# Optimization experiments

Hardware: AMD Instinct MI355X
Metric: run time of the kernel (lower is better)

The kernel has to match this reference:

```python
import jax, jax.numpy as jnp
import numpy as np

D_MODEL = 1024
N_HEADS = 16
HEAD_DIM = 64
INNER = N_HEADS * HEAD_DIM
D_FF = 4096


def ln_novar(x, w, b):
    # mean-only 'layernorm' (no variance division), per original LayerNormNoVar
    u = jnp.mean(x, axis=-1, keepdims=True)
    return w * (x - u) + b


def setup_inputs() -> dict:
    key = jax.random.key(0)
    ks = jax.random.split(key, 12)
    s = lambda k, shape, scale: jax.random.normal(k, shape, dtype=jnp.float32) * scale
    inp = {
        "src": s(ks[0], (4, 2048, D_MODEL), 1.0),
        "pre_norm_w": jnp.ones((D_MODEL,), jnp.float32),
        "pre_norm_b": jnp.zeros((D_MODEL,), jnp.float32),
        "wq": s(ks[1], (D_MODEL, INNER), 0.02),
        "wk": s(ks[2], (D_MODEL, INNER), 0.02),
        "wv": s(ks[3], (D_MODEL, INNER), 0.02),
        "w_proj": s(ks[4], (INNER, D_MODEL), 0.02),
        "b_proj": jnp.zeros((D_MODEL,), jnp.float32),
        "norm1_w": jnp.ones((D_MODEL,), jnp.float32),
        "norm1_b": jnp.zeros((D_MODEL,), jnp.float32),
        "w1": s(ks[5], (D_MODEL, D_FF), 0.02),
        "b1": jnp.zeros((D_FF,), jnp.float32),
        "w2": s(ks[6], (D_FF, D_MODEL), 0.02),
        "b2": jnp.zeros((D_MODEL,), jnp.float32),
    }
    return inp


def reference(src, pre_norm_w, pre_norm_b, wq, wk, wv, w_proj, b_proj,
              norm1_w, norm1_b, w1, b1, w2, b2):
    B, N, _ = src.shape
    scale = HEAD_DIM ** -0.5
    x = ln_novar(src, pre_norm_w, pre_norm_b)
    q = (x @ wq).reshape(B, N, N_HEADS, HEAD_DIM)
    k = (x @ wk).reshape(B, N, N_HEADS, HEAD_DIM)
    v = (x @ wv).reshape(B, N, N_HEADS, HEAD_DIM)
    attn = jnp.einsum('bqhd,bkhd->bhqk', q, k) * scale
    attn = jax.nn.softmax(attn, axis=-1)
    o = jnp.einsum('bhqk,bkhd->bqhd', attn, v).reshape(B, N, INNER)
    o = o @ w_proj + b_proj
    src = src + o
    src = ln_novar(src, norm1_w, norm1_b)
    ff = jax.nn.relu(src @ w1 + b1) @ w2 + b2
    return src + ff
```

## Files before the change

### kernel.cpp

```cpp
#include <hip/hip_runtime.h>
#include <hip/hip_bf16.h>
#include <stdint.h>

typedef __hip_bfloat16 bf16;
typedef float f32x4 __attribute__((ext_vector_type(4)));
typedef float f32x16 __attribute__((ext_vector_type(16)));
typedef short v8s __attribute__((ext_vector_type(8)));
typedef __bf16 v8bf __attribute__((ext_vector_type(8)));
typedef unsigned int v4u __attribute__((ext_vector_type(4)));
typedef unsigned int u32;

static constexpr int MROWS = 8192;
static constexpr int DM    = 1024;
static constexpr int DFF   = 4096;
static constexpr int SEQ   = 2048;

__device__ __forceinline__ f32x4 mfma16(v8s a, v8s b, f32x4 c) {
  return __builtin_amdgcn_mfma_f32_16x16x32_bf16(
      __builtin_bit_cast(v8bf, a), __builtin_bit_cast(v8bf, b), c, 0, 0, 0);
}
__device__ __forceinline__ f32x16 mfma32(v8s a, v8s b, f32x16 c) {
  return __builtin_amdgcn_mfma_f32_32x32x16_bf16(
      __builtin_bit_cast(v8bf, a), __builtin_bit_cast(v8bf, b), c, 0, 0, 0);
}

__device__ __forceinline__ void gload_lds16(const void* g, void* l) {
  __builtin_amdgcn_global_load_lds(
      (const __attribute__((address_space(1))) void*)g,
      (__attribute__((address_space(3))) void*)l, 16, 0, 0);
}

__device__ __forceinline__ u32 cvtpk_bf16(float a, float b) {
  u32 r;
  asm("v_cvt_pk_bf16_f32 %0, %1, %2" : "=v"(r) : "v"(a), "v"(b));
  return r;
}
__device__ __forceinline__ void pl32swap(u32& x, u32& y) {
  asm volatile("v_permlane32_swap_b32 %0, %1" : "+v"(x), "+v"(y));
}
__device__ __forceinline__ float fast_exp2(float x) {
  float r;
  asm("v_exp_f32 %0, %1" : "=v"(r) : "v"(x));
  return r;
}

__global__ __launch_bounds__(256) void transpose_cast(
    const float* __restrict__ W, bf16* __restrict__ WT, int K, int N) {
  __shared__ float tile[32][33];
  const int c0 = blockIdx.x * 32;
  const int r0 = blockIdx.y * 32;
  const int tx = threadIdx.x & 31, ty = threadIdx.x >> 5;
  #pragma unroll
  for (int i = 0; i < 32; i += 8)
    tile[ty + i][tx] = W[(size_t)(r0 + ty + i) * N + c0 + tx];
  __syncthreads();
  #pragma unroll
  for (int i = 0; i < 32; i += 8)
    WT[(size_t)(c0 + ty + i) * K + r0 + tx] = __float2bfloat16(tile[tx][ty + i]);
}

__global__ __launch_bounds__(256) void ln_novar_kernel(
    const float* __restrict__ x, const float* __restrict__ w,
    const float* __restrict__ b, bf16* __restrict__ ob, float* __restrict__ of) {
  const int row = blockIdx.x;
  const int t = threadIdx.x;
  const float4 v = ((const float4*)(x + (size_t)row * DM))[t];
  float s = v.x + v.y + v.z + v.w;
  #pragma unroll
  for (int off = 32; off > 0; off >>= 1) s += __shfl_down(s, off, 64);
  __shared__ float wsum[4];
  if ((t & 63) == 0) wsum[t >> 6] = s;
  __syncthreads();
  const float u = (wsum[0] + wsum[1] + wsum[2] + wsum[3]) * (1.0f / DM);
  const float4 wv = ((const float4*)w)[t];
  const float4 bv = ((const float4*)b)[t];
  const float o0 = wv.x * (v.x - u) + bv.x;
  const float o1 = wv.y * (v.y - u) + bv.y;
  const float o2 = wv.z * (v.z - u) + bv.z;
  const float o3 = wv.w * (v.w - u) + bv.w;
  bf16* op = ob + (size_t)row * DM + t * 4;
  op[0] = __float2bfloat16(o0); op[1] = __float2bfloat16(o1);
  op[2] = __float2bfloat16(o2); op[3] = __float2bfloat16(o3);
  if (of) {
    float4 o4; o4.x = o0; o4.y = o1; o4.z = o2; o4.w = o3;
    ((float4*)(of + (size_t)row * DM))[t] = o4;
  }
}

#define BM 128
#define BN 256
#define BK 64
#define ASZ (BM * BK)
#define BSZ (BN * BK)
template <int EPI>
__global__ __launch_bounds__(512, 2) void gemm_bt(
    const bf16* __restrict__ A, const bf16* __restrict__ BT,
    bf16* __restrict__ Cb, float* __restrict__ Cf,
    const float* __restrict__ bias, const float* __restrict__ res,
    int M, int Nn, int K) {
  __shared__ __align__(16) bf16 S[3][ASZ + BSZ];

  const int tid = threadIdx.x;
  const int lane = tid & 63;
  const int wave = tid >> 6;
  const int wr = wave >> 2;
  const int wcn = wave & 3;

  const int nwg = gridDim.x;
  const int nbx = Nn / BN;
  int bid = (blockIdx.x & 7) * (nwg >> 3) + (blockIdx.x >> 3);
  const int GM = 4;
  const int grp = bid / (GM * nbx);
  const int rem = bid - grp * (GM * nbx);
  const int by = grp * GM + (rem & (GM - 1));
  const int bx = rem >> 2;
  const int tM = by * BM, tN = bx * BN;

  f32x4 acc[4][4] = {};
  const int nk = K / BK;

  auto STAGE = [&](int buf, int kt) {
    const int k0 = kt * BK;
    bf16* Ab = &S[buf][0];
    bf16* Bb = &S[buf][ASZ];
    #pragma unroll
    for (int c = 0; c < 2; ++c) {
      const int slot = c * 512 + tid;
      const int row = slot >> 3, s = slot & 7;
      const int kk = ((s ^ (row & 7)) << 3);
      gload_lds16(A + (size_t)(tM + row) * K + k0 + kk, (void*)(Ab + slot * 8));
    }
    #pragma unroll
    for (int c = 0; c < 4; ++c) {
      const int slot = c * 512 + tid;
      const int row = slot >> 3, s = slot & 7;
      const int kk = ((s ^ (row & 7)) << 3);
      gload_lds16(BT + (size_t)(tN + row) * K + k0 + kk, (void*)(Bb + slot * 8));
    }
  };

  auto LD = [&](v8s* af, v8s* bfr, int buf, int kk) {
    const bf16* Ab = &S[buf][0];
    const bf16* Bb = &S[buf][ASZ];
    const int kslot = kk * 4 + (lane >> 4);
    #pragma unroll
    for (int m = 0; m < 4; ++m) {
      const int row = wr * 64 + m * 16 + (lane & 15);
      af[m] = *(const v8s*)(Ab + (row * 8 + (kslot ^ (row & 7))) * 8);
    }
    #pragma unroll
    for (int n = 0; n < 4; ++n) {
      const int row = wcn * 64 + n * 16 + (lane & 15);
      bfr[n] = *(const v8s*)(Bb + (row * 8 + (kslot ^ (row & 7))) * 8);
    }
  };

  v8s fA0[4], fB0[4], fA1[4], fB1[4];

  STAGE(0, 0);
  STAGE(1, 1);
  asm volatile("s_waitcnt vmcnt(6)" ::: "memory");
  __builtin_amdgcn_s_barrier();
  asm volatile("" ::: "memory");
  LD(fA0, fB0, 0, 0);

  for (int kt = 0; kt < nk; ++kt) {
    const int cur = kt % 3;
    if (kt + 2 < nk) STAGE((kt + 2) % 3, kt + 2);

    LD(fA1, fB1, cur, 1);
    __builtin_amdgcn_s_setprio(1);
    #pragma unroll
    for (int m = 0; m < 4; ++m)
      #pragma unroll
      for (int n = 0; n < 4; ++n)
        acc[m][n] = mfma16(fA0[m], fB0[n], acc[m][n]);
    __builtin_amdgcn_s_setprio(0);

    if (kt + 2 < nk) asm volatile("s_waitcnt vmcnt(6)" ::: "memory");
    else             asm volatile("s_waitcnt vmcnt(0)" ::: "memory");
    __builtin_amdgcn_s_barrier();
    asm volatile("" ::: "memory");

    if (kt + 1 < nk) LD(fA0, fB0, (kt + 1) % 3, 0);
    __builtin_amdgcn_s_setprio(1);
    #pragma unroll
    for (int m = 0; m < 4; ++m)
      #pragma unroll
      for (int n = 0; n < 4; ++n)
        acc[m][n] = mfma16(fA1[m], fB1[n], acc[m][n]);
    __builtin_amdgcn_s_setprio(0);

    asm volatile("" ::: "memory");
    __builtin_amdgcn_s_barrier();
    asm volatile("" ::: "memory");
  }

  #pragma unroll
  for (int m = 0; m < 4; ++m) {
    #pragma unroll
    for (int n = 0; n < 4; ++n) {
      const int row0 = tM + wr * 64 + m * 16 + ((lane >> 4) << 2);
      const int col = tN + wcn * 64 + n * 16 + (lane & 15);
      #pragma unroll
      for (int r = 0; r < 4; ++r) {
        const int row = row0 + r;
        float v = acc[m][n][r];
        if (EPI == 0) {
          Cb[(size_t)row * Nn + col] = __float2bfloat16(v);
        } else if (EPI == 1) {
          v += bias[col];
          v = fmaxf(v, 0.0f);
          Cb[(size_t)row * Nn + col] = __float2bfloat16(v);
        } else if (EPI == 2) {
          v += bias[col] + res[(size_t)row * Nn + col];
          Cf[(size_t)row * Nn + col] = v;
        } else {
          const int sec = tN >> 10;
          if (sec == 0) {
            Cb[(size_t)row * Nn + col] = __float2bfloat16(v);
          } else {
            const int b = row >> 11, nn2 = row & 2047;
            const int ktt = nn2 >> 6, key = nn2 & 63;
            if (sec == 1) {
              const int ck = col - 1024;
              const int h = ck >> 6, dc = (ck >> 3) & 7, e = ck & 7;
              bf16* krp = (bf16*)(void*)bias;
              krp[((size_t)((b * 16 + h) * 32 + ktt)) * 4096 + dc * 512 +
                  key * 8 + e] = __float2bfloat16(v);
            } else {
              const int cv = col - 2048;
              const int h = cv >> 6, d = cv & 63;
              const int kc = key >> 3, e2 = key & 7;
              bf16* vrp = (bf16*)(void*)res;
              vrp[((size_t)((b * 16 + h) * 32 + ktt)) * 4096 + kc * 512 +
                  d * 8 + e2] = __float2bfloat16(v);
            }
          }
        }
      }
    }
  }
}

#define PPV(i) ((i) < 16 ? s0[(i) & 15] : s1[(i) & 15])
__global__ __launch_bounds__(256, 4) void attn_kernel(
    const bf16* __restrict__ qkv, const bf16* __restrict__ krep,
    const bf16* __restrict__ vrep, bf16* __restrict__ ob) {
  const int qt = blockIdx.x & 15;
  const int bh = blockIdx.x >> 4;
  const int b = bh >> 4, h = bh & 15;
  const int tid = threadIdx.x;
  const int lane = tid & 63, wave = tid >> 6;
  const int c = lane & 31, hi = lane >> 5;
  const float CEXP = 0.180336880111120426f;

  __shared__ __align__(16) bf16 Ks[2][4096];
  __shared__ __align__(16) bf16 Vs[2][4096];

  const int qrow = qt * 128 + wave * 32 + c;
  const bf16* qp = qkv + (size_t)(b * SEQ + qrow) * 3072 + h * 64;
  v8s qf[4];
  #pragma unroll
  for (int ks = 0; ks < 4; ++ks)
    qf[ks] = *(const v8s*)(qp + ks * 16 + hi * 8);

  f32x16 o0 = {}, o1 = {};
  float mrow = -1e30f, lrow = 0.0f;

  const size_t tilebase = (size_t)(bh * 32) * 4096;
  #pragma unroll
  for (int j = 0; j < 2; ++j) {
    gload_lds16(krep + tilebase + (tid + j * 256) * 8, &Ks[0][(tid + j * 256) * 8]);
    gload_lds16(vrep + tilebase + (tid + j * 256) * 8, &Vs[0][(tid + j * 256) * 8]);
  }
  asm volatile("s_waitcnt vmcnt(0)" ::: "memory");
  __builtin_amdgcn_s_barrier();
  asm volatile("" ::: "memory");

  for (int kt = 0; kt < 32; ++kt) {
    const int cur = kt & 1;
    if (kt < 31) {
      const size_t nb = tilebase + (size_t)(kt + 1) * 4096;
      #pragma unroll
      for (int j = 0; j < 2; ++j) {
        gload_lds16(krep + nb + (tid + j * 256) * 8, &Ks[cur ^ 1][(tid + j * 256) * 8]);
        gload_lds16(vrep + nb + (tid + j * 256) * 8, &Vs[cur ^ 1][(tid + j * 256) * 8]);
      }
    }
    const bf16* KB = Ks[cur];
    const bf16* VB = Vs[cur];

    f32x16 s0 = {}, s1 = {};
    __builtin_amdgcn_s_setprio(1);
    #pragma unroll
    for (int ks = 0; ks < 4; ++ks) {
      const int ch = (2 * ks + hi) * 512;
      v8s a0 = *(const v8s*)(KB + ch + c * 8);
      v8s a1 = *(const v8s*)(KB + ch + (c + 32) * 8);
      s0 = mfma32(a0, qf[ks], s0);
      s1 = mfma32(a1, qf[ks], s1);
    }
    __builtin_amdgcn_s_setprio(0);

    float mA = -1e30f, mB = -1e30f;
    #pragma unroll
    for (int i = 0; i < 16; i += 2) {
      mA = fmaxf(fmaxf(s0[i], s0[i + 1]), mA);
      mB = fmaxf(fmaxf(s1[i], s1[i + 1]), mB);
    }
    float tmax = fmaxf(mA, mB);
    tmax = fmaxf(tmax, __shfl_xor(tmax, 32, 64));
    if (__any(tmax - mrow > 64.0f)) {
      const float mnew = fmaxf(mrow, tmax);
      const float ef = fast_exp2((mrow - mnew) * CEXP);
      mrow = mnew;
      lrow *= ef;
      #pragma unroll
      for (int r = 0; r < 16; ++r) {
        const float efq = __shfl(ef, (r & 3) + 8 * (r >> 2) + 4 * hi, 64);
        o0[r] *= efq;
        o1[r] *= efq;
      }
    }
    const float nmc = -mrow * CEXP;
    float rs0 = 0.0f, rs1 = 0.0f;
    #pragma unroll
    for (int i = 0; i < 16; ++i) {
      s0[i] = fast_exp2(fmaf(s0[i], CEXP, nmc));
      s1[i] = fast_exp2(fmaf(s1[i], CEXP, nmc));
      rs0 += s0[i];
      rs1 += s1[i];
    }
    float rs = rs0 + rs1;
    rs += __shfl_xor(rs, 32, 64);
    lrow += rs;

    v8s pa[4];
    #pragma unroll
    for (int ks = 0; ks < 4; ++ks) {
      u32 x  = cvtpk_bf16(PPV(8 * ks + 0), PPV(8 * ks + 1));
      u32 y  = cvtpk_bf16(PPV(8 * ks + 4), PPV(8 * ks + 5));
      u32 x2 = cvtpk_bf16(PPV(8 * ks + 2), PPV(8 * ks + 3));
      u32 y2 = cvtpk_bf16(PPV(8 * ks + 6), PPV(8 * ks + 7));
      pl32swap(x, y);
      pl32swap(x2, y2);
      v4u w; w.x = x; w.y = x2; w.z = y; w.w = y2;
      pa[ks] = __builtin_bit_cast(v8s, w);
    }

    __builtin_amdgcn_s_setprio(1);
    #pragma unroll
    for (int ks = 0; ks < 4; ++ks) {
      const int ch = (2 * ks + hi) * 512;
      v8s b0 = *(const v8s*)(VB + ch + c * 8);
      v8s b1 = *(const v8s*)(VB + ch + (c + 32) * 8);
      o0 = mfma32(pa[ks], b0, o0);
      o1 = mfma32(pa[ks], b1, o1);
    }
    __builtin_amdgcn_s_setprio(0);

    asm volatile("s_waitcnt vmcnt(0)" ::: "memory");
    __builtin_amdgcn_s_barrier();
    asm volatile("" ::: "memory");
  }

  const float rl = 1.0f / lrow;
  const size_t orow0 = (size_t)(b * SEQ + qt * 128 + wave * 32);
  #pragma unroll
  for (int r = 0; r < 16; ++r) {
    const int q = (r & 3) + 8 * (r >> 2) + 4 * hi;
    const float rq = __shfl(rl, q, 64);
    bf16* op = ob + (orow0 + q) * DM + h * 64;
    op[c] = __float2bfloat16(o0[r] * rq);
    op[32 + c] = __float2bfloat16(o1[r] * rq);
  }
}

extern "C" void kernel_launch(void* const* d_in, const int* in_sizes, int n_in,
                              void* d_out, int out_size, void* d_ws,
                              size_t ws_size, hipStream_t stream) {
  const float* src   = (const float*)d_in[0];
  const float* pnw   = (const float*)d_in[1];
  const float* pnb   = (const float*)d_in[2];
  const float* wq    = (const float*)d_in[3];
  const float* wk    = (const float*)d_in[4];
  const float* wv    = (const float*)d_in[5];
  const float* wproj = (const float*)d_in[6];
  const float* bproj = (const float*)d_in[7];
  const float* n1w   = (const float*)d_in[8];
  const float* n1b   = (const float*)d_in[9];
  const float* w1    = (const float*)d_in[10];
  const float* b1    = (const float*)d_in[11];
  const float* w2    = (const float*)d_in[12];
  const float* b2    = (const float*)d_in[13];
  float* out = (float*)d_out;

  char* ws = (char*)d_ws;
  size_t off = 0;
  bf16* WTqkv = (bf16*)(ws + off); off += (size_t)3072 * 1024 * 2;
  bf16* WTprj = (bf16*)(ws + off); off += (size_t)1024 * 1024 * 2;
  bf16* WT1   = (bf16*)(ws + off); off += (size_t)4096 * 1024 * 2;
  bf16* WT2   = (bf16*)(ws + off); off += (size_t)1024 * 4096 * 2;
  bf16* xb    = (bf16*)(ws + off); off += (size_t)MROWS * DM * 2;
  bf16* qkvb  = (bf16*)(ws + off); off += (size_t)MROWS * 3072 * 2;
  bf16* obuf  = (bf16*)(ws + off); off += (size_t)MROWS * DM * 2;
  float* yf   = (float*)(ws + off); off += (size_t)MROWS * DM * 4;
  bf16* h1    = (bf16*)(ws + off); off += (size_t)MROWS * DFF * 2;
  bf16* krep = h1;
  bf16* vrep = h1 + (size_t)64 * SEQ * 64;

  const dim3 blk(256);
  const dim3 gblk(512);

  transpose_cast<<<dim3(32, 32), blk, 0, stream>>>(wq, WTqkv, 1024, 1024);
  transpose_cast<<<dim3(32, 32), blk, 0, stream>>>(wk, WTqkv + 1024 * 1024, 1024, 1024);
  transpose_cast<<<dim3(32, 32), blk, 0, stream>>>(wv, WTqkv + 2048 * 1024, 1024, 1024);
  transpose_cast<<<dim3(32, 32), blk, 0, stream>>>(wproj, WTprj, 1024, 1024);
  transpose_cast<<<dim3(128, 32), blk, 0, stream>>>(w1, WT1, 1024, 4096);
  transpose_cast<<<dim3(32, 128), blk, 0, stream>>>(w2, WT2, 4096, 1024);

  ln_novar_kernel<<<MROWS, blk, 0, stream>>>(src, pnw, pnb, xb, nullptr);

  gemm_bt<3><<<dim3((3072 / BN) * (MROWS / BM)), gblk, 0, stream>>>(
      xb, WTqkv, qkvb, nullptr, (const float*)krep, (const float*)vrep,
      MROWS, 3072, 1024);

  attn_kernel<<<dim3(16 * 64), dim3(256), 0, stream>>>(qkvb, krep, vrep, obuf);

  gemm_bt<2><<<dim3((1024 / BN) * (MROWS / BM)), gblk, 0, stream>>>(
      obuf, WTprj, nullptr, yf, bproj, src, MROWS, 1024, 1024);

  ln_novar_kernel<<<MROWS, blk, 0, stream>>>(yf, n1w, n1b, xb, out);

  gemm_bt<1><<<dim3((4096 / BN) * (MROWS / BM)), gblk, 0, stream>>>(
      xb, WT1, h1, nullptr, b1, nullptr, MROWS, 4096, 1024);

  gemm_bt<2><<<dim3((1024 / BN) * (MROWS / BM)), gblk, 0, stream>>>(
      h1, WT2, nullptr, out, b2, out, MROWS, 1024, 4096);
}
```

Baseline: 417.6 us.

## Replace pipelined 128x256 GEMM with simpler 128/64x128 tiles at 256 threads

Rewrites the GEMM kernel to use smaller output tiles (128x128 for the wide QKV and FFN1 GEMMs, 64x128 for the N=1024 GEMMs) with 256-thread blocks. The triple-buffered LDS pipeline is dropped in favour of a plain load, sync, compute loop. The smaller tiles and smaller LDS footprint allow more blocks per CU and more blocks on the narrow GEMMs, aiming for better occupancy and wave balance. In exchange, global loads no longer overlap MFMA work within a block, and data reuse per tile drops.

```diff
diff --git a/kernel.cpp b/kernel.cpp
--- a/kernel.cpp
+++ b/kernel.cpp
@@ -87,121 +87,86 @@
   }
 }
 
-#define BM 128
-#define BN 256
-#define BK 64
-#define ASZ (BM * BK)
-#define BSZ (BN * BK)
-template <int EPI>
-__global__ __launch_bounds__(512, 2) void gemm_bt(
+template <int EPI, int TBM>
+__global__ __launch_bounds__(256) void gemm_bt(
     const bf16* __restrict__ A, const bf16* __restrict__ BT,
     bf16* __restrict__ Cb, float* __restrict__ Cf,
     const float* __restrict__ bias, const float* __restrict__ res,
     int M, int Nn, int K) {
-  __shared__ __align__(16) bf16 S[3][ASZ + BSZ];
+  constexpr int WN = (TBM == 128) ? 2 : 4;
+  constexpr int NW = 4 / (WN / 2) / 2 * 2;
+  constexpr int NFR = (TBM == 128) ? 4 : 2;
+  __shared__ __align__(16) bf16 As[TBM * 64];
+  __shared__ __align__(16) bf16 Bs[128 * 64];
 
   const int tid = threadIdx.x;
   const int lane = tid & 63;
   const int wave = tid >> 6;
-  const int wr = wave >> 2;
-  const int wcn = wave & 3;
+  const int wr = wave / WN;
+  const int wc = wave % WN;
 
   const int nwg = gridDim.x;
-  const int nbx = Nn / BN;
+  const int nbx = Nn / 128;
   int bid = (blockIdx.x & 7) * (nwg >> 3) + (blockIdx.x >> 3);
   const int GM = 4;
   const int grp = bid / (GM * nbx);
   const int rem = bid - grp * (GM * nbx);
   const int by = grp * GM + (rem & (GM - 1));
   const int bx = rem >> 2;
-  const int tM = by * BM, tN = bx * BN;
-
-  f32x4 acc[4][4] = {};
-  const int nk = K / BK;
-
-  auto STAGE = [&](int buf, int kt) {
-    const int k0 = kt * BK;
-    bf16* Ab = &S[buf][0];
-    bf16* Bb = &S[buf][ASZ];
-    #pragma unroll
-    for (int c = 0; c < 2; ++c) {
-      const int slot = c * 512 + tid;
+  const int tM = by * TBM, tN = bx * 128;
+
+  f32x4 acc[4][NFR] = {};
+  const int nk = K / 64;
+
+  for (int kt = 0; kt < nk; ++kt) {
+    if (kt) __syncthreads();
+    const int k0 = kt * 64;
+    #pragma unroll
+    for (int c = 0; c < TBM / 32; ++c) {
+      const int slot = c * 256 + tid;
       const int row = slot >> 3, s = slot & 7;
       const int kk = ((s ^ (row & 7)) << 3);
-      gload_lds16(A + (size_t)(tM + row) * K + k0 + kk, (void*)(Ab + slot * 8));
+      gload_lds16(A + (size_t)(tM + row) * K + k0 + kk, (void*)(As + slot * 8));
     }
     #pragma unroll
     for (int c = 0; c < 4; ++c) {
-      const int slot = c * 512 + tid;
+      const int slot = c * 256 + tid;
       const int row = slot >> 3, s = slot & 7;
       const int kk = ((s ^ (row & 7)) << 3);
-      gload_lds16(BT + (size_t)(tN + row) * K + k0 + kk, (void*)(Bb + slot * 8));
-    }
-  };
-
-  auto LD = [&](v8s* af, v8s* bfr, int buf, int kk) {
-    const bf16* Ab = &S[buf][0];
-    const bf16* Bb = &S[buf][ASZ];
-    const int kslot = kk * 4 + (lane >> 4);
-    #pragma unroll
-    for (int m = 0; m < 4; ++m) {
-      const int row = wr * 64 + m * 16 + (lane & 15);
-      af[m] = *(const v8s*)(Ab + (row * 8 + (kslot ^ (row & 7))) * 8);
-    }
-    #pragma unroll
-    for (int n = 0; n < 4; ++n) {
-      const int row = wcn * 64 + n * 16 + (lane & 15);
-      bfr[n] = *(const v8s*)(Bb + (row * 8 + (kslot ^ (row & 7))) * 8);
-    }
-  };
-
-  v8s fA0[4], fB0[4], fA1[4], fB1[4];
-
-  STAGE(0, 0);
-  STAGE(1, 1);
-  asm volatile("s_waitcnt vmcnt(6)" ::: "memory");
-  __builtin_amdgcn_s_barrier();
-  asm volatile("" ::: "memory");
-  LD(fA0, fB0, 0, 0);
-
-  for (int kt = 0; kt < nk; ++kt) {
-    const int cur = kt % 3;
-    if (kt + 2 < nk) STAGE((kt + 2) % 3, kt + 2);
-
-    LD(fA1, fB1, cur, 1);
-    __builtin_amdgcn_s_setprio(1);
-    #pragma unroll
-    for (int m = 0; m < 4; ++m)
-      #pragma unroll
-      for (int n = 0; n < 4; ++n)
-        acc[m][n] = mfma16(fA0[m], fB0[n], acc[m][n]);
-    __builtin_amdgcn_s_setprio(0);
-
-    if (kt + 2 < nk) asm volatile("s_waitcnt vmcnt(6)" ::: "memory");
-    else             asm volatile("s_waitcnt vmcnt(0)" ::: "memory");
-    __builtin_amdgcn_s_barrier();
-    asm volatile("" ::: "memory");
-
-    if (kt + 1 < nk) LD(fA0, fB0, (kt + 1) % 3, 0);
-    __builtin_amdgcn_s_setprio(1);
-    #pragma unroll
-    for (int m = 0; m < 4; ++m)
-      #pragma unroll
-      for (int n = 0; n < 4; ++n)
-        acc[m][n] = mfma16(fA1[m], fB1[n], acc[m][n]);
-    __builtin_amdgcn_s_setprio(0);
-
-    asm volatile("" ::: "memory");
-    __builtin_amdgcn_s_barrier();
-    asm volatile("" ::: "memory");
+      gload_lds16(BT + (size_t)(tN + row) * K + k0 + kk, (void*)(Bs + slot * 8));
+    }
+    __syncthreads();
+
+    #pragma unroll
+    for (int kk = 0; kk < 2; ++kk) {
+      const int kslot = kk * 4 + (lane >> 4);
+      v8s af[4], bfr[NFR];
+      #pragma unroll
+      for (int m = 0; m < 4; ++m) {
+        const int row = wr * 64 + m * 16 + (lane & 15);
+        af[m] = *(const v8s*)(As + (row * 8 + (kslot ^ (row & 7))) * 8);
+      }
+      #pragma unroll
+      for (int n = 0; n < NFR; ++n) {
+        const int row = wc * (128 / WN) + n * 16 + (lane & 15);
+        bfr[n] = *(const v8s*)(Bs + (row * 8 + (kslot ^ (row & 7))) * 8);
+      }
+      __builtin_amdgcn_s_setprio(1);
+      #pragma unroll
+      for (int m = 0; m < 4; ++m)
+        #pragma unroll
+        for (int n = 0; n < NFR; ++n)
+          acc[m][n] = mfma16(af[m], bfr[n], acc[m][n]);
+      __builtin_amdgcn_s_setprio(0);
+    }
   }
 
   #pragma unroll
   for (int m = 0; m < 4; ++m) {
     #pragma unroll
-    for (int n = 0; n < 4; ++n) {
+    for (int n = 0; n < NFR; ++n) {
       const int row0 = tM + wr * 64 + m * 16 + ((lane >> 4) << 2);
-      const int col = tN + wcn * 64 + n * 16 + (lane & 15);
+      const int col = tN + wc * (128 / WN) + n * 16 + (lane & 15);
       #pragma unroll
       for (int r = 0; r < 4; ++r) {
         const int row = row0 + r;
@@ -411,7 +376,6 @@
   bf16* vrep = h1 + (size_t)64 * SEQ * 64;
 
   const dim3 blk(256);
-  const dim3 gblk(512);
 
   transpose_cast<<<dim3(32, 32), blk, 0, stream>>>(wq, WTqkv, 1024, 1024);
   transpose_cast<<<dim3(32, 32), blk, 0, stream>>>(wk, WTqkv + 1024 * 1024, 1024, 1024);
@@ -422,20 +386,20 @@
 
   ln_novar_kernel<<<MROWS, blk, 0, stream>>>(src, pnw, pnb, xb, nullptr);
 
-  gemm_bt<3><<<dim3((3072 / BN) * (MROWS / BM)), gblk, 0, stream>>>(
+  gemm_bt<3, 128><<<dim3((3072 / 128) * (MROWS / 128)), blk, 0, stream>>>(
       xb, WTqkv, qkvb, nullptr, (const float*)krep, (const float*)vrep,
       MROWS, 3072, 1024);
 
   attn_kernel<<<dim3(16 * 64), dim3(256), 0, stream>>>(qkvb, krep, vrep, obuf);
 
-  gemm_bt<2><<<dim3((1024 / BN) * (MROWS / BM)), gblk, 0, stream>>>(
+  gemm_bt<2, 64><<<dim3((1024 / 128) * (MROWS / 64)), blk, 0, stream>>>(
       obuf, WTprj, nullptr, yf, bproj, src, MROWS, 1024, 1024);
 
   ln_novar_kernel<<<MROWS, blk, 0, stream>>>(yf, n1w, n1b, xb, out);
 
-  gemm_bt<1><<<dim3((4096 / BN) * (MROWS / BM)), gblk, 0, stream>>>(
+  gemm_bt<1, 128><<<dim3((4096 / 128) * (MROWS / 128)), blk, 0, stream>>>(
       xb, WT1, h1, nullptr, b1, nullptr, MROWS, 4096, 1024);
 
-  gemm_bt<2><<<dim3((1024 / BN) * (MROWS / BM)), gblk, 0, stream>>>(
+  gemm_bt<2, 64><<<dim3((1024 / 128) * (MROWS / 64)), blk, 0, stream>>>(
       h1, WT2, nullptr, out, b2, out, MROWS, 1024, 4096);
 }
```

New measurement: 420.6 us. About the same (+0.7%).
